# Performance work log

Hardware: AMD Instinct MI355X
Metric: run time of the kernel (lower is better)

The kernel has to match this reference:

```python
import jax, jax.numpy as jnp
import numpy as np

COST_CLASS, COST_BBOX, COST_GIOU = 1.0, 5.0, 2.0


def box_cxcywh_to_xyxy(b):
    cx, cy, w, h = jnp.split(b, 4, axis=-1)
    return jnp.concatenate([cx - 0.5 * w, cy - 0.5 * h, cx + 0.5 * w, cy + 0.5 * h], axis=-1)


def generalized_box_iou(a, b):
    # a: [N,4], b: [T,4] in xyxy -> [N,T]
    area_a = (a[:, 2] - a[:, 0]) * (a[:, 3] - a[:, 1])
    area_b = (b[:, 2] - b[:, 0]) * (b[:, 3] - b[:, 1])
    lt = jnp.maximum(a[:, None, :2], b[None, :, :2])
    rb = jnp.minimum(a[:, None, 2:], b[None, :, 2:])
    wh = jnp.clip(rb - lt, 0.0)
    inter = wh[..., 0] * wh[..., 1]
    union = area_a[:, None] + area_b[None, :] - inter
    iou = inter / union
    lt_e = jnp.minimum(a[:, None, :2], b[None, :, :2])
    rb_e = jnp.maximum(a[:, None, 2:], b[None, :, 2:])
    wh_e = jnp.clip(rb_e - lt_e, 0.0)
    area_e = wh_e[..., 0] * wh_e[..., 1]
    return iou - (area_e - union) / area_e


def cost_matrix(pred_logits, pred_boxes, tgt_labels, tgt_boxes):
    B, Q, _ = pred_logits.shape
    probs = jax.nn.softmax(pred_logits.reshape(B * Q, -1), axis=-1)
    pb = pred_boxes.reshape(B * Q, 4)
    tl = tgt_labels.reshape(-1)
    tb = tgt_boxes.reshape(-1, 4)
    cc = -probs[:, tl]                                              # [BQ, BM]
    cb = jnp.sum(jnp.abs(pb[:, None, :] - tb[None, :, :]), axis=-1)  # L1 cdist
    cg = -generalized_box_iou(box_cxcywh_to_xyxy(pb), box_cxcywh_to_xyxy(tb))
    C = COST_CLASS * cc + COST_BBOX * cb + COST_GIOU * cg
    return C.reshape(B, Q, -1)


def hungarian(cost):
    # Jonker-Volgenant shortest-augmenting-path assignment.
    # cost: [n, m] with n <= m; returns the column assigned to each row, [n] int32.
    n, m = cost.shape
    INF = jnp.float32(1e30)

    def solve_row(i, uvp):
        u, v, p = uvp  # u:[n+1] row potentials (+dummy), v:[m+1], p:[m+1] row assigned per col
        p = p.at[m].set(i)  # virtual start column m holds the new row
        state = (jnp.int32(m), u, v, p,
                 jnp.full(m + 1, INF, jnp.float32),   # minv
                 jnp.zeros(m + 1, bool),              # used
                 jnp.zeros(m + 1, jnp.int32))         # way

        def cond(s):
            j0, _, _, p, _, _, _ = s
            return p[j0] != -1

        def body(s):
            j0, u, v, p, minv, used, way = s
            used = used.at[j0].set(True)
            i0 = p[j0]
            cur = jnp.where(used[:m], INF, cost[i0] - u[i0] - v[:m])
            better = cur < minv[:m]
            minv = minv.at[:m].set(jnp.where(better, cur, minv[:m]))
            way = way.at[:m].set(jnp.where(better, j0, way[:m]))
            masked = jnp.where(used[:m], INF, minv[:m])
            j1 = jnp.argmin(masked).astype(jnp.int32)
            delta = masked[j1]
            u = u.at[jnp.where(used, p, n)].add(jnp.where(used, delta, 0.0))
            v = jnp.where(used, v - delta, v)
            minv = jnp.where(used, minv, minv - delta)
            return (j1, u, v, p, minv, used, way)

        j0, u, v, p, minv, used, way = jax.lax.while_loop(cond, body, state)

        def a_cond(s):
            return s[0] != m

        def a_body(s):
            j0, p = s
            j1 = way[j0]
            return (j1, p.at[j0].set(p[j1]))

        _, p = jax.lax.while_loop(a_cond, a_body, (j0, p))
        return (u, v, p)

    u0 = jnp.zeros(n + 1, jnp.float32)
    v0 = jnp.zeros(m + 1, jnp.float32)
    p0 = jnp.full(m + 1, -1, jnp.int32)
    _, _, p = jax.lax.fori_loop(0, n, solve_row, (u0, v0, p0))
    row_of_col = p[:m]
    cols = jnp.arange(m, dtype=jnp.int32)
    col_of_row = jnp.zeros(n + 1, jnp.int32).at[
        jnp.where(row_of_col >= 0, row_of_col, n)].set(cols)
    return col_of_row[:n]


def setup_inputs() -> dict:
    key = jax.random.key(0)
    k1, k2, k3, k4 = jax.random.split(key, 4)
    B, Q, NCLS, M = 32, 300, 92, 50
    return {
        'pred_logits': jax.random.normal(k1, (B, Q, NCLS), jnp.float32),
        'pred_boxes': jax.random.uniform(k2, (B, Q, 4), dtype=jnp.float32),
        'tgt_labels': jax.random.randint(k3, (B, M), 0, NCLS),
        'tgt_boxes': jax.random.uniform(k4, (B, M, 4), dtype=jnp.float32),
    }


def reference(pred_logits, pred_boxes, tgt_labels, tgt_boxes):
    B, Q, _ = pred_logits.shape
    M = tgt_labels.shape[1]
    C = cost_matrix(pred_logits, pred_boxes, tgt_labels, tgt_boxes)  # [B, Q, B*M]
    # per-image block of columns: C[i, :, i*M:(i+1)*M]
    C4 = C.reshape(B, Q, B, M)
    C_per = jnp.transpose(jnp.diagonal(C4, axis1=0, axis2=2), (2, 0, 1))  # [B, Q, M]
    q = jax.vmap(hungarian)(jnp.transpose(C_per, (0, 2, 1)))  # [B, M]: query per target
    order = jnp.argsort(q, axis=1).astype(jnp.int32)
    pred_idx = jnp.take_along_axis(q, order, axis=1)  # sorted query indices
    gt_idx = order                                     # matching target indices
    return pred_idx, gt_idx, C
```

## Files before the change

### kernel.cpp

```cpp
#include <hip/hip_runtime.h>
#include <hip/hip_bf16.h>

#define NB   32
#define NQ   300
#define NCLS 92
#define NM   50
#define BM   (NB * NM)
#define BQ   (NB * NQ)
#define HM   NQ
#define HN   NM
#define PITCH 305
#define BIG  1e30f
#define HUNG_BLOCKS NB
#define COST_ROWS_PER_BLOCK 16
#define COST_BLOCKS (BQ / COST_ROWS_PER_BLOCK)
#define NBLOCKS (HUNG_BLOCKS + COST_BLOCKS)

typedef float vf4 __attribute__((ext_vector_type(4)));

#define FENCE() __threadfence_block()

__device__ __forceinline__ float wred_max(float v) {
#pragma unroll
  for (int m = 1; m < 64; m <<= 1) v = fmaxf(v, __shfl_xor(v, m, 64));
  return v;
}
__device__ __forceinline__ float wred_sum(float v) {
#pragma unroll
  for (int m = 1; m < 64; m <<= 1) v += __shfl_xor(v, m, 64);
  return v;
}
__device__ __forceinline__ float wred_min(float v) {
#pragma unroll
  for (int m = 1; m < 64; m <<= 1) v = fminf(v, __shfl_xor(v, m, 64));
  return v;
}

__device__ __forceinline__ float pair_cost(float ax1, float ay1, float ax2,
                                           float ay2, float areaA,
                                           const float4& pb, const float4& t,
                                           float negprob) {
  float cb = fabsf(pb.x - t.x) + fabsf(pb.y - t.y) +
             fabsf(pb.z - t.z) + fabsf(pb.w - t.w);
  float bx1 = t.x - 0.5f * t.z, by1 = t.y - 0.5f * t.w;
  float bx2 = t.x + 0.5f * t.z, by2 = t.y + 0.5f * t.w;
  float areaB = (bx2 - bx1) * (by2 - by1);
  float iw = fmaxf(fminf(ax2, bx2) - fmaxf(ax1, bx1), 0.f);
  float ih = fmaxf(fminf(ay2, by2) - fmaxf(ay1, by1), 0.f);
  float inter = iw * ih;
  float uni = areaA + areaB - inter;
  float iou = inter / uni;
  float ew = fmaxf(fmaxf(ax2, bx2) - fminf(ax1, bx1), 0.f);
  float eh = fmaxf(fmaxf(ay2, by2) - fminf(ay1, by1), 0.f);
  float areaE = ew * eh;
  float giou = iou - (areaE - uni) / areaE;
  return (negprob + 5.f * cb) - 2.f * giou;
}

__device__ __forceinline__ void wave_softmax(const float* __restrict__ lrow,
                                             float* prow, int lane) {
  float x0 = (lane < NCLS) ? lrow[lane] : -BIG;
  float x1 = (lane + 64 < NCLS) ? lrow[lane + 64] : -BIG;
  float mx = wred_max(fmaxf(x0, x1));
  float e0 = expf(x0 - mx), e1 = expf(x1 - mx);
  float s = wred_sum(e0 + e1);
  if (lane < NCLS) prow[lane] = e0 / s;
  if (lane + 64 < NCLS) prow[lane + 64] = e1 / s;
  FENCE();
}

__global__ __launch_bounds__(1024) void fused_kernel(
    const float* __restrict__ logits, const float* __restrict__ pboxes,
    const int* __restrict__ tlab, const float* __restrict__ tbox,
    float* __restrict__ outp) {
  __shared__ float hc[HN * PITCH];
  __shared__ float probs_s[16][NCLS];
  __shared__ float u[HN + 1];
  __shared__ int   p[HM + 1];
  __shared__ int   way[HM];
  __shared__ int   am[HN];
  __shared__ int   pend[HN];
  __shared__ int   qarr[HN];

  float* C = outp + 2 * BM;
  int tid = threadIdx.x, wave = tid >> 6, lane = tid & 63;

  if (blockIdx.x >= HUNG_BLOCKS) {
    int row = (blockIdx.x - HUNG_BLOCKS) * COST_ROWS_PER_BLOCK + wave;
    wave_softmax(logits + (size_t)row * NCLS, probs_s[wave], lane);

    float4 pb = reinterpret_cast<const float4*>(pboxes)[row];
    float ax1 = pb.x - 0.5f * pb.z, ay1 = pb.y - 0.5f * pb.w;
    float ax2 = pb.x + 0.5f * pb.z, ay2 = pb.y + 0.5f * pb.w;
    float areaA = (ax2 - ax1) * (ay2 - ay1);

    const float4* tbv = reinterpret_cast<const float4*>(tbox);
    const int4*   tlv = reinterpret_cast<const int4*>(tlab);
    vf4* crow = reinterpret_cast<vf4*>(C + (size_t)row * BM);
    for (int q4 = lane; q4 < BM / 4; q4 += 64) {
      int4 cls = tlv[q4];
      int clsa[4] = {cls.x, cls.y, cls.z, cls.w};
      vf4 o;
#pragma unroll
      for (int e = 0; e < 4; e++) {
        float4 t = tbv[q4 * 4 + e];
        o[e] = pair_cost(ax1, ay1, ax2, ay2, areaA, pb, t,
                         -probs_s[wave][clsa[e]]);
      }
      __builtin_nontemporal_store(o, &crow[q4]);
    }
    return;
  }

  int b = blockIdx.x;

  for (int x = tid; x <= HM; x += 1024) p[x] = -1;
  if (tid == 0) u[HN] = 0.f;

  float4 t_reg = make_float4(0.f, 0.f, 0.f, 0.f);
  int cls_reg = 0;
  if (lane < NM) {
    t_reg = reinterpret_cast<const float4*>(tbox)[b * NM + lane];
    cls_reg = tlab[b * NM + lane];
  }

  const float4* pbv = reinterpret_cast<const float4*>(pboxes);
  for (int q = wave; q < NQ; q += 16) {
    wave_softmax(logits + (size_t)(b * NQ + q) * NCLS, probs_s[wave], lane);
    float4 pb = pbv[b * NQ + q];
    float ax1 = pb.x - 0.5f * pb.z, ay1 = pb.y - 0.5f * pb.w;
    float ax2 = pb.x + 0.5f * pb.z, ay2 = pb.y + 0.5f * pb.w;
    float areaA = (ax2 - ax1) * (ay2 - ay1);
    if (lane < NM) {
      float negp = -probs_s[wave][cls_reg];
      hc[lane * PITCH + q] =
          pair_cost(ax1, ay1, ax2, ay2, areaA, pb, t_reg, negp);
    }
  }
  __syncthreads();
  if (wave != 0) return;


  if (lane < HN) {
    float mn = BIG; int amv = 0;
    for (int j = 0; j < HM; j++) {
      float vv = hc[lane * PITCH + j];
      if (vv < mn) { mn = vv; amv = j; }
    }
    u[lane] = mn; am[lane] = amv;
  }
  FENCE();

  int npend = 0;
  for (int i = 0; i < HN; i++) {
    int jm = am[i];
    if (p[jm] == -1) p[jm] = i;
    else pend[npend++] = i;
  }
  FENCE();

  float v_r[5], minv_r[5];
#pragma unroll
  for (int k = 0; k < 5; k++) v_r[k] = 0.f;

  for (int t = 0; t < npend; t++) {
    int i_start = pend[t];
    unsigned usedbits = 0;
#pragma unroll
    for (int k = 0; k < 5; k++) minv_r[k] = BIG;
    if (lane == 0) p[HM] = i_start;
    FENCE();

    int j0 = HM;
    while (true) {
      int i0 = p[j0];
      float ui0 = u[i0];
      if (lane == (j0 & 63)) usedbits |= 1u << (j0 >> 6);

      float best = BIG; int bj = 0;
#pragma unroll
      for (int k = 0; k < 5; k++) {
        int j = lane + 64 * k;
        if (j < HM && !((usedbits >> k) & 1u)) {
          float cur = hc[i0 * PITCH + j] - ui0 - v_r[k];
          if (cur < minv_r[k]) { minv_r[k] = cur; way[j] = j0; }
          if (minv_r[k] < best) { best = minv_r[k]; bj = j; }
        }
      }
      float wmin = wred_min(best);
      unsigned long long ball = __ballot(best == wmin);
      int src = (int)__ffsll((long long)ball) - 1;
      int j1 = __shfl(bj, src, 64);
      float delta = wmin;

#pragma unroll
      for (int k = 0; k < 5; k++) {
        int j = lane + 64 * k;
        if (j <= HM) {
          if ((usedbits >> k) & 1u) {
            v_r[k] -= delta;
            u[p[j]] += delta;
          } else if (j < HM) {
            minv_r[k] -= delta;
          }
        }
      }
      FENCE();
      j0 = j1;
      if (p[j0] == -1) break;
    }

    int jj = j0;
    while (jj != HM) {
      int jn = way[jj];
      p[jj] = p[jn];
      jj = jn;
    }
    FENCE();
  }

  for (int j = lane; j < HM; j += 64) {
    int r = p[j];
    if (r >= 0) qarr[r] = j;
  }
  FENCE();
  if (lane < HN) {
    int qi = qarr[lane];
    int rank = 0;
    for (int t = 0; t < HN; t++) rank += (qarr[t] < qi);
    outp[(size_t)b * NM + rank] = (float)qi;
    outp[BM + (size_t)b * NM + rank] = (float)lane;
  }
}

extern "C" void kernel_launch(void* const* d_in, const int* in_sizes, int n_in,
                              void* d_out, int out_size, void* d_ws, size_t ws_size,
                              hipStream_t stream) {
  const float* logits = (const float*)d_in[0];
  const float* pboxes = (const float*)d_in[1];
  const int*   tlab   = (const int*)d_in[2];
  const float* tbox   = (const float*)d_in[3];
  float* out = (float*)d_out;

  fused_kernel<<<dim3(NBLOCKS), dim3(1024), 0, stream>>>(
      logits, pboxes, tlab, tbox, out);
}
```

Before: 128.9 us.

## Keep Hungarian solver state in registers with wave shuffles instead of LDS

Moves the Hungarian solver's row potentials, column assignments, way pointers and pending list from shared memory into per-lane registers. These values are now read and written with wave shuffles and bitmasks, and the separate used-column bitmap becomes a used-row mask for the potential update. The aim is to cut LDS traffic and fence overhead on the serial augmenting-path loop, which runs in a single wave per image. The trade-off is extra select and shuffle work per step and higher register pressure.

```diff
diff --git a/kernel.cpp b/kernel.cpp
--- a/kernel.cpp
+++ b/kernel.cpp
@@ -34,6 +34,13 @@
 #pragma unroll
   for (int m = 1; m < 64; m <<= 1) v = fminf(v, __shfl_xor(v, m, 64));
   return v;
+}
+
+__device__ __forceinline__ int sel5i(const int* a, int k) {
+  int r = a[0];
+#pragma unroll
+  for (int t = 1; t < 5; t++) r = (k == t) ? a[t] : r;
+  return r;
 }
 
 __device__ __forceinline__ float pair_cost(float ax1, float ay1, float ax2,
@@ -75,11 +82,6 @@
     float* __restrict__ outp) {
   __shared__ float hc[HN * PITCH];
   __shared__ float probs_s[16][NCLS];
-  __shared__ float u[HN + 1];
-  __shared__ int   p[HM + 1];
-  __shared__ int   way[HM];
-  __shared__ int   am[HN];
-  __shared__ int   pend[HN];
   __shared__ int   qarr[HN];
 
   float* C = outp + 2 * BM;
@@ -113,9 +115,6 @@
   }
 
   int b = blockIdx.x;
-
-  for (int x = tid; x <= HM; x += 1024) p[x] = -1;
-  if (tid == 0) u[HN] = 0.f;
 
   float4 t_reg = make_float4(0.f, 0.f, 0.f, 0.f);
   int cls_reg = 0;
@@ -141,49 +140,57 @@
   if (wave != 0) return;
 
 
+  float u_reg = 0.f;
+  int am_reg = 0;
   if (lane < HN) {
     float mn = BIG; int amv = 0;
     for (int j = 0; j < HM; j++) {
       float vv = hc[lane * PITCH + j];
       if (vv < mn) { mn = vv; amv = j; }
     }
-    u[lane] = mn; am[lane] = amv;
-  }
-  FENCE();
-
-  int npend = 0;
+    u_reg = mn; am_reg = amv;
+  }
+
+  int p_r[5];
+#pragma unroll
+  for (int k = 0; k < 5; k++) p_r[k] = -1;
+  unsigned long long pending = 0;
   for (int i = 0; i < HN; i++) {
-    int jm = am[i];
-    if (p[jm] == -1) p[jm] = i;
-    else pend[npend++] = i;
-  }
-  FENCE();
+    int jm = __shfl(am_reg, i, 64);
+    int kk = jm >> 6, ll = jm & 63;
+    int cur = __shfl(sel5i(p_r, kk), ll, 64);
+    if (cur == -1) {
+#pragma unroll
+      for (int k = 0; k < 5; k++)
+        if (k == kk && lane == ll) p_r[k] = i;
+    } else {
+      pending |= 1ull << i;
+    }
+  }
 
   float v_r[5], minv_r[5];
+  int way_r[5];
 #pragma unroll
   for (int k = 0; k < 5; k++) v_r[k] = 0.f;
 
-  for (int t = 0; t < npend; t++) {
-    int i_start = pend[t];
-    unsigned usedbits = 0;
+  while (pending) {
+    int i_start = (int)__ffsll((long long)pending) - 1;
+    pending &= pending - 1;
 #pragma unroll
     for (int k = 0; k < 5; k++) minv_r[k] = BIG;
-    if (lane == 0) p[HM] = i_start;
-    FENCE();
-
-    int j0 = HM;
+    unsigned usedc = 0;
+    unsigned long long used_rows = 1ull << i_start;
+    int i0 = i_start, j0 = HM, jfree = -1;
+
     while (true) {
-      int i0 = p[j0];
-      float ui0 = u[i0];
-      if (lane == (j0 & 63)) usedbits |= 1u << (j0 >> 6);
-
+      float ui0 = __shfl(u_reg, i0, 64);
       float best = BIG; int bj = 0;
 #pragma unroll
       for (int k = 0; k < 5; k++) {
         int j = lane + 64 * k;
-        if (j < HM && !((usedbits >> k) & 1u)) {
+        if (j < HM && !((usedc >> k) & 1u)) {
           float cur = hc[i0 * PITCH + j] - ui0 - v_r[k];
-          if (cur < minv_r[k]) { minv_r[k] = cur; way[j] = j0; }
+          if (cur < minv_r[k]) { minv_r[k] = cur; way_r[k] = j0; }
           if (minv_r[k] < best) { best = minv_r[k]; bj = j; }
         }
       }
@@ -193,35 +200,46 @@
       int j1 = __shfl(bj, src, 64);
       float delta = wmin;
 
+      if ((used_rows >> lane) & 1ull) u_reg += delta;
 #pragma unroll
       for (int k = 0; k < 5; k++) {
         int j = lane + 64 * k;
-        if (j <= HM) {
-          if ((usedbits >> k) & 1u) {
-            v_r[k] -= delta;
-            u[p[j]] += delta;
-          } else if (j < HM) {
-            minv_r[k] -= delta;
-          }
+        if (j < HM) {
+          if ((usedc >> k) & 1u) v_r[k] -= delta;
+          else                   minv_r[k] -= delta;
         }
       }
-      FENCE();
+      int k1 = j1 >> 6, l1 = j1 & 63;
+      if (lane == l1) usedc |= 1u << k1;
+      int psel = __shfl(sel5i(p_r, k1), l1, 64);
+      if (psel == -1) { jfree = j1; break; }
+      i0 = psel;
+      used_rows |= 1ull << i0;
       j0 = j1;
-      if (p[j0] == -1) break;
-    }
-
-    int jj = j0;
-    while (jj != HM) {
-      int jn = way[jj];
-      p[jj] = p[jn];
-      jj = jn;
-    }
-    FENCE();
-  }
-
-  for (int j = lane; j < HM; j += 64) {
-    int r = p[j];
-    if (r >= 0) qarr[r] = j;
+    }
+
+    int jj = jfree;
+    while (true) {
+      int kk = jj >> 6, ll = jj & 63;
+      int wsel = __shfl(sel5i(way_r, kk), ll, 64);
+      int pv;
+      if (wsel == HM) {
+        pv = i_start;
+      } else {
+        pv = __shfl(sel5i(p_r, wsel >> 6), wsel & 63, 64);
+      }
+#pragma unroll
+      for (int k = 0; k < 5; k++)
+        if (k == kk && lane == ll) p_r[k] = pv;
+      if (wsel == HM) break;
+      jj = wsel;
+    }
+  }
+
+#pragma unroll
+  for (int k = 0; k < 5; k++) {
+    int j = lane + 64 * k;
+    if (j < HM && p_r[k] >= 0) qarr[p_r[k]] = j;
   }
   FENCE();
   if (lane < HN) {
```

Result: slower. 136.8 us (+6.1%).
